# Kernel tuning notes

Measured on AMD Instinct MI355X. Metric: run time of the kernel, lower is better.

The kernel has to match this reference:

```python
import jax, jax.numpy as jnp
import numpy as np

WINDOW_SIZE = 16
DILATION = 2

B, L, H, E = 2, 4096, 8, 64


def setup_inputs() -> dict:
    key = jax.random.key(0)
    kq, kk, kv = jax.random.split(key, 3)
    queries = jax.random.normal(kq, (B, L, H, E), dtype=jnp.float32)
    keys = jax.random.normal(kk, (B, L, H, E), dtype=jnp.float32)
    values = jax.random.normal(kv, (B, L, H, E), dtype=jnp.float32)
    return {"queries": queries, "keys": keys, "values": values}


def _window_indices(Lk: int):
    # offsets: [-r, ..., r] * dilation ; idx[l, w] = clamp(l + off[w], 0, Lk-1)
    offsets = jnp.arange(-WINDOW_SIZE, WINDOW_SIZE + 1) * DILATION
    idx = jnp.arange(Lk)[:, None] + offsets[None, :]
    return jnp.clip(idx, 0, Lk - 1)


def reference(queries, keys, values):
    # queries/keys/values: [B, L, H, E]
    Bq, Lq, Hq, Eq = queries.shape
    scale = 1.0 / jnp.sqrt(jnp.asarray(Eq, queries.dtype))
    idx = _window_indices(keys.shape[1])
    K_win = keys[:, idx]
    V_win = values[:, idx]
    scores = jnp.einsum('blhe,blwhe->blhw', queries, K_win) * scale
    A = jax.nn.softmax(scores, axis=-1)
    V = jnp.einsum('blhw,blwhe->blhe', A, V_win)    # [B, L, H, E]
    return V
```

## Files before the change

### kernel.cpp

```cpp
#include <hip/hip_runtime.h>
#include <hip/hip_bf16.h>
#include <math.h>

#define B_    2
#define L_    4096
#define H_    8
#define E_    64
#define TILE  64
#define KROWS 128
#define QSTR  72
#define KSTR  72
#define VTSTR 136
#define PSTR  136

using frag8 = __attribute__((ext_vector_type(8))) short;
using fl4   = __attribute__((ext_vector_type(4))) float;

__device__ __forceinline__ unsigned short f2bf(float f) {
    return __builtin_bit_cast(unsigned short, __float2bfloat16(f));
}

__global__ __launch_bounds__(256, 3)
void lda_kernel(const float* __restrict__ Q, const float* __restrict__ K,
                const float* __restrict__ V, float* __restrict__ O) {
    __shared__ unsigned short U[TILE * PSTR];
    __shared__ unsigned short Ks[KROWS * KSTR];
    __shared__ unsigned short Vt[E_ * VTSTR];

    const int tid  = threadIdx.x;
    const int lane = tid & 63;
    const int wave = tid >> 6;
    const int col  = lane & 15;
    const int quad = lane >> 4;
    const int l0   = blockIdx.x * TILE;
    const int bh   = blockIdx.y;
    const int b    = bh >> 3;
    const int h    = bh & 7;

    const size_t base = ((size_t)(b * L_) * H_ + h) * E_;
    const int    rs   = H_ * E_;

    #pragma unroll
    for (int i = 0; i < 4; ++i) {
        int idx = tid + 256 * i;
        int row = idx >> 4, c4 = idx & 15;
        float4 v = *(const float4*)(Q + base + (size_t)(l0 + row) * rs + c4 * 4);
        uint2 p;
        p.x = (unsigned)f2bf(v.x) | ((unsigned)f2bf(v.y) << 16);
        p.y = (unsigned)f2bf(v.z) | ((unsigned)f2bf(v.w) << 16);
        *(uint2*)&U[row * QSTR + c4 * 4] = p;
    }
    #pragma unroll
    for (int i = 0; i < 8; ++i) {
        int idx = tid + 256 * i;
        int row = idx >> 4, c4 = idx & 15;
        int rg  = l0 - 32 + row;
        rg = rg < 0 ? 0 : (rg > L_ - 1 ? L_ - 1 : rg);
        float4 v = *(const float4*)(K + base + (size_t)rg * rs + c4 * 4);
        uint2 p;
        p.x = (unsigned)f2bf(v.x) | ((unsigned)f2bf(v.y) << 16);
        p.y = (unsigned)f2bf(v.z) | ((unsigned)f2bf(v.w) << 16);
        *(uint2*)&Ks[row * KSTR + c4 * 4] = p;
    }
    #pragma unroll
    for (int p = 0; p < 8; ++p) {
        int rb = p * 16 + wave * 4;
        float a0, a1, a2, a3;
        {
            int rg = l0 - 32 + rb;     rg = rg < 0 ? 0 : (rg > L_-1 ? L_-1 : rg);
            a0 = V[base + (size_t)rg * rs + lane];
        }
        {
            int rg = l0 - 32 + rb + 1; rg = rg < 0 ? 0 : (rg > L_-1 ? L_-1 : rg);
            a1 = V[base + (size_t)rg * rs + lane];
        }
        {
            int rg = l0 - 32 + rb + 2; rg = rg < 0 ? 0 : (rg > L_-1 ? L_-1 : rg);
            a2 = V[base + (size_t)rg * rs + lane];
        }
        {
            int rg = l0 - 32 + rb + 3; rg = rg < 0 ? 0 : (rg > L_-1 ? L_-1 : rg);
            a3 = V[base + (size_t)rg * rs + lane];
        }
        uint2 u;
        u.x = (unsigned)f2bf(a0) | ((unsigned)f2bf(a1) << 16);
        u.y = (unsigned)f2bf(a2) | ((unsigned)f2bf(a3) << 16);
        *(uint2*)&Vt[lane * VTSTR + rb] = u;
    }
    __syncthreads();

    frag8 aq[2];
    #pragma unroll
    for (int k = 0; k < 2; ++k)
        aq[k] = *(const frag8*)&U[(wave * 16 + col) * QSTR + k * 32 + quad * 8];

    fl4 S[5];
    #pragma unroll
    for (int t = 0; t < 5; ++t) {
        int nt = wave + t;
        fl4 c = {0.f, 0.f, 0.f, 0.f};
        #pragma unroll
        for (int k = 0; k < 2; ++k) {
            frag8 bk = *(const frag8*)&Ks[(nt * 16 + col) * KSTR + k * 32 + quad * 8];
            c = __builtin_amdgcn_mfma_f32_16x16x32_bf16(aq[k], bk, c, 0, 0, 0);
        }
        S[t] = c;
    }

    float pv[5][4];
    #pragma unroll
    for (int reg = 0; reg < 4; ++reg) {
        float mx = -1e30f;
        #pragma unroll
        for (int t = 0; t < 5; ++t) {
            int d = t * 16 + col - quad * 4 - reg;
            bool ib = (d >= 0) && (d <= 64) && ((d & 1) == 0);
            float sv = S[t][reg] * 0.125f;
            if (ib) mx = fmaxf(mx, sv);
        }
        #pragma unroll
        for (int m = 1; m < 16; m <<= 1) mx = fmaxf(mx, __shfl_xor(mx, m));
        float sum = 0.f;
        #pragma unroll
        for (int t = 0; t < 5; ++t) {
            int d = t * 16 + col - quad * 4 - reg;
            bool ib = (d >= 0) && (d <= 64) && ((d & 1) == 0);
            float e = ib ? __expf(S[t][reg] * 0.125f - mx) : 0.f;
            pv[t][reg] = e;
            sum += e;
        }
        #pragma unroll
        for (int m = 1; m < 16; m <<= 1) sum += __shfl_xor(sum, m);
        float inv = 1.f / sum;
        #pragma unroll
        for (int t = 0; t < 5; ++t) pv[t][reg] *= inv;
    }
    __syncthreads();

    #pragma unroll
    for (int i = 0; i < 5; ++i) {
        int idx = tid + 256 * i;
        if (idx < (TILE * PSTR) / 8) {
            uint4 z = {0u, 0u, 0u, 0u};
            *(uint4*)&U[idx * 8] = z;
        }
    }
    __syncthreads();

    #pragma unroll
    for (int reg = 0; reg < 4; ++reg) {
        int l = wave * 16 + quad * 4 + reg;
        #pragma unroll
        for (int t = 0; t < 5; ++t) {
            int r = (wave + t) * 16 + col;
            int d = r - l;
            if ((d >= 0) && (d <= 64) && ((d & 1) == 0))
                U[l * PSTR + r] = f2bf(pv[t][reg]);
        }
    }
    __syncthreads();

    frag8 ap[4];
    #pragma unroll
    for (int k = 0; k < 4; ++k)
        ap[k] = *(const frag8*)&U[(wave * 16 + col) * PSTR + k * 32 + quad * 8];

    #pragma unroll
    for (int nt = 0; nt < 4; ++nt) {
        fl4 c = {0.f, 0.f, 0.f, 0.f};
        #pragma unroll
        for (int k = 0; k < 4; ++k) {
            frag8 bv = *(const frag8*)&Vt[(nt * 16 + col) * VTSTR + k * 32 + quad * 8];
            c = __builtin_amdgcn_mfma_f32_16x16x32_bf16(ap[k], bv, c, 0, 0, 0);
        }
        #pragma unroll
        for (int reg = 0; reg < 4; ++reg) {
            int l = wave * 16 + quad * 4 + reg;
            O[base + (size_t)(l0 + l) * rs + nt * 16 + col] = c[reg];
        }
    }
}

extern "C" void kernel_launch(void* const* d_in, const int* in_sizes, int n_in,
                              void* d_out, int out_size, void* d_ws, size_t ws_size,
                              hipStream_t stream) {
    const float* Q = (const float*)d_in[0];
    const float* K = (const float*)d_in[1];
    const float* V = (const float*)d_in[2];
    float* O = (float*)d_out;

    dim3 grid(L_ / TILE, B_ * H_);
    dim3 block(256);
    lda_kernel<<<grid, block, 0, stream>>>(Q, K, V, O);
}
```

Baseline: 97.00 us.

## Split queries by dilation parity to shrink windowed MFMA work and LDS

Queries and keys are split by parity (even/odd positions), so each wave handles 16 same-parity queries against 48 same-parity keys. This removes the half of the score and PV MFMAs that the dilation mask would otherwise zero out. Q and K are now loaded straight from global memory into registers instead of staged in LDS, and each wave writes its P tile to a private LDS region, which drops most block-wide barriers. LDS use falls and occupancy is raised to 4 blocks per SM. The cost is redundant global K reads across waves and gathers with a stride of two rows.

```diff
diff --git a/kernel.cpp b/kernel.cpp
--- a/kernel.cpp
+++ b/kernel.cpp
@@ -6,12 +6,8 @@
 #define L_    4096
 #define H_    8
 #define E_    64
-#define TILE  64
-#define KROWS 128
-#define QSTR  72
-#define KSTR  72
 #define VTSTR 136
-#define PSTR  136
+#define PSTR  72
 
 using frag8 = __attribute__((ext_vector_type(8))) short;
 using fl4   = __attribute__((ext_vector_type(4))) float;
@@ -19,20 +15,29 @@
 __device__ __forceinline__ unsigned short f2bf(float f) {
     return __builtin_bit_cast(unsigned short, __float2bfloat16(f));
 }
+__device__ __forceinline__ frag8 pack8(float4 a, float4 b) {
+    frag8 r;
+    r[0] = (short)f2bf(a.x); r[1] = (short)f2bf(a.y);
+    r[2] = (short)f2bf(a.z); r[3] = (short)f2bf(a.w);
+    r[4] = (short)f2bf(b.x); r[5] = (short)f2bf(b.y);
+    r[6] = (short)f2bf(b.z); r[7] = (short)f2bf(b.w);
+    return r;
+}
 
-__global__ __launch_bounds__(256, 3)
+__global__ __launch_bounds__(256, 4)
 void lda_kernel(const float* __restrict__ Q, const float* __restrict__ K,
                 const float* __restrict__ V, float* __restrict__ O) {
-    __shared__ unsigned short U[TILE * PSTR];
-    __shared__ unsigned short Ks[KROWS * KSTR];
     __shared__ unsigned short Vt[E_ * VTSTR];
+    __shared__ unsigned short Pw[4 * 16 * PSTR];
 
     const int tid  = threadIdx.x;
     const int lane = tid & 63;
     const int wave = tid >> 6;
     const int col  = lane & 15;
     const int quad = lane >> 4;
-    const int l0   = blockIdx.x * TILE;
+    const int p    = wave & 1;
+    const int t    = wave >> 1;
+    const int l0   = blockIdx.x * 64;
     const int bh   = blockIdx.y;
     const int b    = bh >> 3;
     const int h    = bh & 7;
@@ -41,141 +46,119 @@
     const int    rs   = H_ * E_;
 
     #pragma unroll
-    for (int i = 0; i < 4; ++i) {
-        int idx = tid + 256 * i;
-        int row = idx >> 4, c4 = idx & 15;
-        float4 v = *(const float4*)(Q + base + (size_t)(l0 + row) * rs + c4 * 4);
-        uint2 p;
-        p.x = (unsigned)f2bf(v.x) | ((unsigned)f2bf(v.y) << 16);
-        p.y = (unsigned)f2bf(v.z) | ((unsigned)f2bf(v.w) << 16);
-        *(uint2*)&U[row * QSTR + c4 * 4] = p;
-    }
-    #pragma unroll
     for (int i = 0; i < 8; ++i) {
-        int idx = tid + 256 * i;
-        int row = idx >> 4, c4 = idx & 15;
-        int rg  = l0 - 32 + row;
-        rg = rg < 0 ? 0 : (rg > L_ - 1 ? L_ - 1 : rg);
-        float4 v = *(const float4*)(K + base + (size_t)rg * rs + c4 * 4);
-        uint2 p;
-        p.x = (unsigned)f2bf(v.x) | ((unsigned)f2bf(v.y) << 16);
-        p.y = (unsigned)f2bf(v.z) | ((unsigned)f2bf(v.w) << 16);
-        *(uint2*)&Ks[row * KSTR + c4 * 4] = p;
-    }
-    #pragma unroll
-    for (int p = 0; p < 8; ++p) {
-        int rb = p * 16 + wave * 4;
+        int g   = wave * 8 + i;
+        int pg  = g >> 4;
+        int rh0 = (g & 15) * 4;
         float a0, a1, a2, a3;
         {
-            int rg = l0 - 32 + rb;     rg = rg < 0 ? 0 : (rg > L_-1 ? L_-1 : rg);
+            int rg = l0 - 32 + 2 * (rh0 + 0) + pg; rg = rg < 0 ? 0 : (rg > L_-1 ? L_-1 : rg);
             a0 = V[base + (size_t)rg * rs + lane];
         }
         {
-            int rg = l0 - 32 + rb + 1; rg = rg < 0 ? 0 : (rg > L_-1 ? L_-1 : rg);
+            int rg = l0 - 32 + 2 * (rh0 + 1) + pg; rg = rg < 0 ? 0 : (rg > L_-1 ? L_-1 : rg);
             a1 = V[base + (size_t)rg * rs + lane];
         }
         {
-            int rg = l0 - 32 + rb + 2; rg = rg < 0 ? 0 : (rg > L_-1 ? L_-1 : rg);
+            int rg = l0 - 32 + 2 * (rh0 + 2) + pg; rg = rg < 0 ? 0 : (rg > L_-1 ? L_-1 : rg);
             a2 = V[base + (size_t)rg * rs + lane];
         }
         {
-            int rg = l0 - 32 + rb + 3; rg = rg < 0 ? 0 : (rg > L_-1 ? L_-1 : rg);
+            int rg = l0 - 32 + 2 * (rh0 + 3) + pg; rg = rg < 0 ? 0 : (rg > L_-1 ? L_-1 : rg);
             a3 = V[base + (size_t)rg * rs + lane];
         }
         uint2 u;
         u.x = (unsigned)f2bf(a0) | ((unsigned)f2bf(a1) << 16);
         u.y = (unsigned)f2bf(a2) | ((unsigned)f2bf(a3) << 16);
-        *(uint2*)&Vt[lane * VTSTR + rb] = u;
+        *(uint2*)&Vt[lane * VTSTR + pg * 64 + rh0] = u;
     }
-    __syncthreads();
 
+    const int lq = l0 + 2 * (16 * t + col) + p;
     frag8 aq[2];
     #pragma unroll
-    for (int k = 0; k < 2; ++k)
-        aq[k] = *(const frag8*)&U[(wave * 16 + col) * QSTR + k * 32 + quad * 8];
+    for (int k = 0; k < 2; ++k) {
+        const float* qp = Q + base + (size_t)lq * rs + k * 32 + quad * 8;
+        aq[k] = pack8(*(const float4*)qp, *(const float4*)(qp + 4));
+    }
 
-    fl4 S[5];
+    fl4 S[3];
     #pragma unroll
-    for (int t = 0; t < 5; ++t) {
-        int nt = wave + t;
-        fl4 c = {0.f, 0.f, 0.f, 0.f};
+    for (int c = 0; c < 3; ++c) {
+        int rhat = 16 * (t + c) + col;
+        int rg = l0 - 32 + 2 * rhat + p;
+        rg = rg < 0 ? 0 : (rg > L_ - 1 ? L_ - 1 : rg);
+        const float* kp = K + base + (size_t)rg * rs;
+        fl4 acc = {0.f, 0.f, 0.f, 0.f};
         #pragma unroll
         for (int k = 0; k < 2; ++k) {
-            frag8 bk = *(const frag8*)&Ks[(nt * 16 + col) * KSTR + k * 32 + quad * 8];
-            c = __builtin_amdgcn_mfma_f32_16x16x32_bf16(aq[k], bk, c, 0, 0, 0);
+            frag8 bk = pack8(*(const float4*)(kp + k * 32 + quad * 8),
+                             *(const float4*)(kp + k * 32 + quad * 8 + 4));
+            acc = __builtin_amdgcn_mfma_f32_16x16x32_bf16(aq[k], bk, acc, 0, 0, 0);
         }
-        S[t] = c;
+        S[c] = acc;
     }
 
-    float pv[5][4];
+    float pw[3][4];
     #pragma unroll
     for (int reg = 0; reg < 4; ++reg) {
+        int off = quad * 4 + reg;
         float mx = -1e30f;
         #pragma unroll
-        for (int t = 0; t < 5; ++t) {
-            int d = t * 16 + col - quad * 4 - reg;
-            bool ib = (d >= 0) && (d <= 64) && ((d & 1) == 0);
-            float sv = S[t][reg] * 0.125f;
-            if (ib) mx = fmaxf(mx, sv);
+        for (int c = 0; c < 3; ++c) {
+            int j = 16 * c + col - off;
+            if (j >= 0 && j <= 32) mx = fmaxf(mx, S[c][reg] * 0.125f);
         }
         #pragma unroll
         for (int m = 1; m < 16; m <<= 1) mx = fmaxf(mx, __shfl_xor(mx, m));
         float sum = 0.f;
         #pragma unroll
-        for (int t = 0; t < 5; ++t) {
-            int d = t * 16 + col - quad * 4 - reg;
-            bool ib = (d >= 0) && (d <= 64) && ((d & 1) == 0);
-            float e = ib ? __expf(S[t][reg] * 0.125f - mx) : 0.f;
-            pv[t][reg] = e;
-            sum += e;
+        for (int c = 0; c < 3; ++c) {
+            int j = 16 * c + col - off;
+            float e = (j >= 0 && j <= 32) ? __expf(S[c][reg] * 0.125f - mx) : 0.f;
+            pw[c][reg] = e; sum += e;
         }
         #pragma unroll
         for (int m = 1; m < 16; m <<= 1) sum += __shfl_xor(sum, m);
         float inv = 1.f / sum;
         #pragma unroll
-        for (int t = 0; t < 5; ++t) pv[t][reg] *= inv;
+        for (int c = 0; c < 3; ++c) pw[c][reg] *= inv;
     }
-    __syncthreads();
 
+    const int pb = wave * 16 * PSTR;
     #pragma unroll
-    for (int i = 0; i < 5; ++i) {
-        int idx = tid + 256 * i;
-        if (idx < (TILE * PSTR) / 8) {
-            uint4 z = {0u, 0u, 0u, 0u};
-            *(uint4*)&U[idx * 8] = z;
+    for (int i = 0; i < 3; ++i) {
+        int idx = lane + 64 * i;
+        if (idx < 144) { uint4 z = {0u,0u,0u,0u}; *(uint4*)&Pw[pb + idx * 8] = z; }
+    }
+    #pragma unroll
+    for (int reg = 0; reg < 4; ++reg) {
+        int off = quad * 4 + reg;
+        #pragma unroll
+        for (int c = 0; c < 3; ++c) {
+            int j = 16 * c + col - off;
+            if (j >= 0 && j <= 32)
+                Pw[pb + off * PSTR + 16 * (t + c) + col] = f2bf(pw[c][reg]);
         }
     }
+
+    frag8 ap[2];
+    #pragma unroll
+    for (int k = 0; k < 2; ++k)
+        ap[k] = *(const frag8*)&Pw[pb + col * PSTR + k * 32 + quad * 8];
+
     __syncthreads();
-
-    #pragma unroll
-    for (int reg = 0; reg < 4; ++reg) {
-        int l = wave * 16 + quad * 4 + reg;
-        #pragma unroll
-        for (int t = 0; t < 5; ++t) {
-            int r = (wave + t) * 16 + col;
-            int d = r - l;
-            if ((d >= 0) && (d <= 64) && ((d & 1) == 0))
-                U[l * PSTR + r] = f2bf(pv[t][reg]);
-        }
-    }
-    __syncthreads();
-
-    frag8 ap[4];
-    #pragma unroll
-    for (int k = 0; k < 4; ++k)
-        ap[k] = *(const frag8*)&U[(wave * 16 + col) * PSTR + k * 32 + quad * 8];
 
     #pragma unroll
     for (int nt = 0; nt < 4; ++nt) {
         fl4 c = {0.f, 0.f, 0.f, 0.f};
         #pragma unroll
-        for (int k = 0; k < 4; ++k) {
-            frag8 bv = *(const frag8*)&Vt[(nt * 16 + col) * VTSTR + k * 32 + quad * 8];
+        for (int k = 0; k < 2; ++k) {
+            frag8 bv = *(const frag8*)&Vt[(nt * 16 + col) * VTSTR + p * 64 + k * 32 + quad * 8];
             c = __builtin_amdgcn_mfma_f32_16x16x32_bf16(ap[k], bv, c, 0, 0, 0);
         }
         #pragma unroll
         for (int reg = 0; reg < 4; ++reg) {
-            int l = wave * 16 + quad * 4 + reg;
+            int l = 2 * (16 * t + quad * 4 + reg) + p;
             O[base + (size_t)(l0 + l) * rs + nt * 16 + col] = c[reg];
         }
     }
@@ -189,7 +172,7 @@
     const float* V = (const float*)d_in[2];
     float* O = (float*)d_out;
 
-    dim3 grid(L_ / TILE, B_ * H_);
+    dim3 grid(L_ / 64, B_ * H_);
     dim3 block(256);
     lda_kernel<<<grid, block, 0, stream>>>(Q, K, V, O);
 }
```

Result: no change. 95.67 us (-1.4%).
